# Optimization experiments

Hardware: AMD Instinct MI355X
Metric: run time of the kernel (lower is better)

## Reference

```python
import jax, jax.numpy as jnp
import numpy as np

VOCAB = 50000
D = 128      # word_embedding_size
H = 64       # attention_hidden_dim


def _doc_embed(words, emb_table, w_self, b_self):
    """words: (..., W) int -> (..., D) via tanh self-attention pooling over words."""
    we = emb_table[words]                                # (..., W, D)
    scores = jnp.tanh(we @ w_self + b_self)              # (..., W, 1)
    wgt = jax.nn.softmax(scores, axis=-2)                # softmax over word dim
    return jnp.sum(wgt * we, axis=-2)                    # (..., D)


def _attention(reviews_emb, query_emb, Wq, bq, w_red):
    """reviews_emb: (B,R,D), query_emb: (B,1,D) -> (B,D)."""
    B = query_emb.shape[0]
    pq = jnp.tanh(query_emb.reshape(B, D) @ Wq + bq)     # (B, D*H)
    pq = pq.reshape(B, D, H)
    s = jnp.einsum('brd,bdh->brh', reviews_emb, pq)      # (B,R,H)
    r = s @ w_red                                        # (B,R,1)
    w = jax.nn.softmax(r, axis=1)                        # softmax over reviews
    return jnp.sum(w * reviews_emb, axis=1)              # (B,D)


def setup_inputs() -> dict:
    key = jax.random.key(0)
    ks = jax.random.split(key, 9)
    B, R, W = 256, 20, 100
    user = jax.random.randint(ks[0], (B, R, W), 0, VOCAB)
    item = jax.random.randint(ks[1], (B, R, W), 0, VOCAB)
    query = jax.random.randint(ks[2], (B, W), 0, VOCAB)
    emb_table = jax.random.normal(ks[3], (VOCAB, D), dtype=jnp.float32) * 0.01
    w_self = jax.random.normal(ks[4], (D, 1), dtype=jnp.float32) * (1.0 / np.sqrt(D))
    b_self = jax.random.uniform(ks[5], (1,), dtype=jnp.float32, maxval=0.01)
    Wq = jax.random.normal(ks[6], (D, D * H), dtype=jnp.float32) * (1.0 / np.sqrt(D))
    bq = jax.random.uniform(ks[7], (D * H,), dtype=jnp.float32, maxval=0.01)
    w_red = jax.random.normal(ks[8], (H, 1), dtype=jnp.float32) * (1.0 / np.sqrt(H))
    pf = jnp.float32(0.5)  # personalized_factor
    return {"user_reviews_words": user, "item_reviews_words": item, "query": query,
            "emb_table": emb_table, "w_self": w_self, "b_self": b_self,
            "Wq": Wq, "bq": bq, "w_red": w_red, "pf": pf}


def reference(user_reviews_words, item_reviews_words, query,
              emb_table, w_self, b_self, Wq, bq, w_red, pf):
    # mode == 'test'
    user_emb = _doc_embed(user_reviews_words, emb_table, w_self, b_self)   # (B,R,D)
    item_emb = _doc_embed(item_reviews_words, emb_table, w_self, b_self)   # (B,R,D)
    q_emb = _doc_embed(query[:, None, :], emb_table, w_self, b_self)       # (B,1,D)
    user_entity = _attention(user_emb, q_emb, Wq, bq, w_red)               # (B,D)
    item_entity = _attention(item_emb, q_emb, Wq, bq, w_red)               # (B,D)
    personalized = user_entity + pf * q_emb[:, 0, :]
    return (personalized, item_entity)
```

## Files before the change

### kernel.cpp

```cpp
#include <hip/hip_runtime.h>
#include <math.h>

#define D 128
#define H 64
#define W 100
#define R 20
#define NB 256
#define NDOC_UI (NB * R)
#define VOCAB 50000

__device__ __forceinline__ float fast_tanh(float x) {
    float u = __expf(2.0f * x);
    return 1.0f - 2.0f * __builtin_amdgcn_rcpf(1.0f + u);
}
__device__ __forceinline__ float fast_exp_tanh(float x) {
    return __expf(fast_tanh(x));
}

__device__ __forceinline__ unsigned short f2bf(float f) {
    unsigned int b = __float_as_uint(f);
    b += 0x7fffu + ((b >> 16) & 1u);
    return (unsigned short)(b >> 16);
}

__global__ __launch_bounds__(256) void vocab_prep_kernel(
    const float* __restrict__ emb, const float* __restrict__ w_self,
    const float* __restrict__ b_self,
    ushort* __restrict__ emb_bf, float* __restrict__ evocab)
{
    int tid = threadIdx.x, lane32 = tid & 31, grp = tid >> 5;
    int row = blockIdx.x * 8 + grp;
    float4 v   = ((const float4*)emb)[row * 32 + lane32];
    float4 ws4 = ((const float4*)w_self)[lane32];
    float p = v.x * ws4.x + v.y * ws4.y + v.z * ws4.z + v.w * ws4.w;
    p += __shfl_xor(p, 16, 64);
    p += __shfl_xor(p, 8, 64);
    p += __shfl_xor(p, 4, 64);
    p += __shfl_xor(p, 2, 64);
    p += __shfl_xor(p, 1, 64);
    float e = __expf(tanhf(p + b_self[0]));
    if (lane32 == 0) evocab[row] = e;
    ushort4 u;
    u.x = f2bf(v.x * e); u.y = f2bf(v.y * e);
    u.z = f2bf(v.z * e); u.w = f2bf(v.w * e);
    ((ushort4*)emb_bf)[row * 32 + lane32] = u;
}

__global__ __launch_bounds__(256) void doc_embed_bf16_kernel(
    const int* __restrict__ user_w, const int* __restrict__ item_w,
    const int* __restrict__ query_w,
    const ushort* __restrict__ emb_bf, const float* __restrict__ evocab,
    float* __restrict__ user_emb, float* __restrict__ item_emb,
    float* __restrict__ q_emb)
{
    int tid    = threadIdx.x;
    int lane32 = tid & 31;
    int grp    = tid >> 5;
    int doc    = blockIdx.x * 8 + grp;

    const int* wp; float* outp;
    if (doc < NDOC_UI)        { wp = user_w + doc * W;               outp = user_emb + doc * D; }
    else if (doc < 2*NDOC_UI) { int t = doc - NDOC_UI;   wp = item_w  + t * W; outp = item_emb + t * D; }
    else                      { int t = doc - 2*NDOC_UI; wp = query_w + t * W; outp = q_emb    + t * D; }

    int wreg[4];
    #pragma unroll
    for (int k = 0; k < 4; ++k) {
        int idx = k * 32 + lane32;
        wreg[k] = wp[idx > W - 1 ? W - 1 : idx];
    }

    float ep = 0.f;
    #pragma unroll
    for (int k = 0; k < 4; ++k) {
        float e = evocab[wreg[k]];
        if (k < 3 || lane32 < 4) ep += e;
    }
    ep += __shfl_xor(ep, 16, 64);
    ep += __shfl_xor(ep, 8, 64);
    ep += __shfl_xor(ep, 4, 64);
    ep += __shfl_xor(ep, 2, 64);
    ep += __shfl_xor(ep, 1, 64);
    float inv = 1.f / ep;

    int permbase = (tid & 32) << 2;
    int sub      = lane32 >> 4;
    int quad     = lane32 & 15;

    float acc[8];
    #pragma unroll
    for (int j = 0; j < 8; ++j) acc[j] = 0.f;

    const uint4* ebf4 = (const uint4*)emb_bf;

    #pragma unroll
    for (int k = 0; k < 3; ++k) {
        #pragma unroll
        for (int hc = 0; hc < 2; ++hc) {
            int wid[8]; uint4 v[8];
            #pragma unroll
            for (int j = 0; j < 8; ++j) {
                int src = (hc * 8 + j) * 2 + sub;
                wid[j] = __builtin_amdgcn_ds_bpermute(permbase | (src << 2), wreg[k]);
            }
            #pragma unroll
            for (int j = 0; j < 8; ++j)
                v[j] = ebf4[(size_t)(unsigned)wid[j] * 16 + quad];
            #pragma unroll
            for (int j = 0; j < 8; ++j) {
                uint4 x = v[j];
                acc[0] += __uint_as_float(x.x << 16);
                acc[1] += __uint_as_float(x.x & 0xffff0000u);
                acc[2] += __uint_as_float(x.y << 16);
                acc[3] += __uint_as_float(x.y & 0xffff0000u);
                acc[4] += __uint_as_float(x.z << 16);
                acc[5] += __uint_as_float(x.z & 0xffff0000u);
                acc[6] += __uint_as_float(x.w << 16);
                acc[7] += __uint_as_float(x.w & 0xffff0000u);
            }
        }
    }
    {
        int wid[2]; uint4 v[2];
        #pragma unroll
        for (int j = 0; j < 2; ++j) {
            int src = j * 2 + sub;
            wid[j] = __builtin_amdgcn_ds_bpermute(permbase | (src << 2), wreg[3]);
        }
        #pragma unroll
        for (int j = 0; j < 2; ++j)
            v[j] = ebf4[(size_t)(unsigned)wid[j] * 16 + quad];
        #pragma unroll
        for (int j = 0; j < 2; ++j) {
            uint4 x = v[j];
            acc[0] += __uint_as_float(x.x << 16);
            acc[1] += __uint_as_float(x.x & 0xffff0000u);
            acc[2] += __uint_as_float(x.y << 16);
            acc[3] += __uint_as_float(x.y & 0xffff0000u);
            acc[4] += __uint_as_float(x.z << 16);
            acc[5] += __uint_as_float(x.z & 0xffff0000u);
            acc[6] += __uint_as_float(x.w << 16);
            acc[7] += __uint_as_float(x.w & 0xffff0000u);
        }
    }

    #pragma unroll
    for (int j = 0; j < 8; ++j) acc[j] += __shfl_xor(acc[j], 16, 64);

    if (lane32 < 16) {
        float4 o0 = make_float4(acc[0]*inv, acc[1]*inv, acc[2]*inv, acc[3]*inv);
        float4 o1 = make_float4(acc[4]*inv, acc[5]*inv, acc[6]*inv, acc[7]*inv);
        ((float4*)outp)[quad * 2]     = o0;
        ((float4*)outp)[quad * 2 + 1] = o1;
    }
}

__global__ __launch_bounds__(256, 7) void doc_embed_fp32_kernel(
    const int* __restrict__ user_w, const int* __restrict__ item_w,
    const int* __restrict__ query_w,
    const float* __restrict__ emb, const float* __restrict__ w_self,
    const float* __restrict__ b_self,
    float* __restrict__ user_emb, float* __restrict__ item_emb,
    float* __restrict__ q_emb)
{
    int tid    = threadIdx.x;
    int lane32 = tid & 31;
    int grp    = tid >> 5;
    int doc    = blockIdx.x * 8 + grp;

    const int* wp; float* outp;
    if (doc < NDOC_UI)        { wp = user_w + doc * W;               outp = user_emb + doc * D; }
    else if (doc < 2*NDOC_UI) { int t = doc - NDOC_UI;   wp = item_w  + t * W; outp = item_emb + t * D; }
    else                      { int t = doc - 2*NDOC_UI; wp = query_w + t * W; outp = q_emb    + t * D; }

    int wreg[4];
    #pragma unroll
    for (int k = 0; k < 4; ++k) {
        int idx = k * 32 + lane32;
        wreg[k] = wp[idx > W - 1 ? W - 1 : idx];
    }

    float4 ws4 = ((const float4*)w_self)[lane32];
    float  bs  = b_self[0];
    const float4* emb4 = (const float4*)emb;
    int permbase = (tid & 32) * 4;

    float4 acc  = make_float4(0.f, 0.f, 0.f, 0.f);
    float  esum = 0.f;

    #pragma unroll
    for (int c = 0; c < 10; ++c) {
        int word[10];
        #pragma unroll
        for (int j = 0; j < 10; ++j) {
            int w = c * 10 + j;
            word[j] = __builtin_amdgcn_ds_bpermute(permbase | ((w & 31) * 4),
                                                   wreg[w >> 5]);
        }
        float4 v[10];
        #pragma unroll
        for (int j = 0; j < 10; ++j)
            v[j] = emb4[(size_t)word[j] * 32 + lane32];

        #pragma unroll
        for (int j = 0; j < 10; ++j) {
            float p = v[j].x * ws4.x + v[j].y * ws4.y + v[j].z * ws4.z + v[j].w * ws4.w;
            p += __shfl_xor(p, 16, 64);
            p += __shfl_xor(p, 8, 64);
            p += __shfl_xor(p, 4, 64);
            p += __shfl_xor(p, 2, 64);
            p += __shfl_xor(p, 1, 64);
            float e = fast_exp_tanh(p + bs);
            esum += e;
            acc.x += e * v[j].x;
            acc.y += e * v[j].y;
            acc.z += e * v[j].z;
            acc.w += e * v[j].w;
        }
    }

    float inv = 1.0f / esum;
    acc.x *= inv; acc.y *= inv; acc.z *= inv; acc.w *= inv;
    ((float4*)outp)[lane32] = acc;
}

__global__ __launch_bounds__(256) void pv_kernel(
    const float* __restrict__ q_emb, const float* __restrict__ Wq,
    const float* __restrict__ bq, const float* __restrict__ w_red,
    float* __restrict__ pv)
{
    __shared__ __align__(16) float qs[64 * 132];
    __shared__ __align__(16) float Wb[128 * 68];

    int dd  = blockIdx.x;
    int m0g = blockIdx.y * 64;
    int tid = threadIdx.x;

    {
        int rrow = tid >> 4;
        int f4   = tid & 15;
        #pragma unroll
        for (int pass = 0; pass < 4; ++pass) {
            int m = pass * 16 + rrow;
            float4 vq = ((const float4*)q_emb)[(m0g + m) * 32 + f4];
            *(float4*)&qs[m * 132 + f4 * 4] = vq;
        }
        #pragma unroll
        for (int pass = 0; pass < 8; ++pass) {
            int k = pass * 16 + rrow;
            float4 vw = ((const float4*)Wq)[k * 2048 + dd * 16 + f4];
            *(float4*)&Wb[k * 68 + f4 * 4] = vw;
        }
    }
    __syncthreads();

    int nthr = tid & 7;
    int mthr = tid >> 3;
    int n0 = nthr * 8;
    int m0 = mthr * 2;

    float acc[2][8];
    #pragma unroll
    for (int i = 0; i < 2; ++i)
        #pragma unroll
        for (int j = 0; j < 8; ++j) acc[i][j] = 0.f;

    for (int k = 0; k < 128; ++k) {
        float4 b0 = *(const float4*)&Wb[k * 68 + n0];
        float4 b1 = *(const float4*)&Wb[k * 68 + n0 + 4];
        float a0 = qs[(m0 + 0) * 132 + k];
        float a1 = qs[(m0 + 1) * 132 + k];
        float bv[8] = {b0.x, b0.y, b0.z, b0.w, b1.x, b1.y, b1.z, b1.w};
        #pragma unroll
        for (int j = 0; j < 8; ++j) {
            acc[0][j] += a0 * bv[j];
            acc[1][j] += a1 * bv[j];
        }
    }

    float4 bqa = ((const float4*)bq)[dd * 16 + nthr * 2];
    float4 bqb = ((const float4*)bq)[dd * 16 + nthr * 2 + 1];
    float4 wra = ((const float4*)w_red)[nthr * 2];
    float4 wrb = ((const float4*)w_red)[nthr * 2 + 1];
    float bqv[8] = {bqa.x, bqa.y, bqa.z, bqa.w, bqb.x, bqb.y, bqb.z, bqb.w};
    float wrv[8] = {wra.x, wra.y, wra.z, wra.w, wrb.x, wrb.y, wrb.z, wrb.w};

    #pragma unroll
    for (int i = 0; i < 2; ++i) {
        float s = 0.f;
        #pragma unroll
        for (int j = 0; j < 8; ++j)
            s += fast_tanh(acc[i][j] + bqv[j]) * wrv[j];
        s += __shfl_xor(s, 1, 64);
        s += __shfl_xor(s, 2, 64);
        s += __shfl_xor(s, 4, 64);
        if (nthr == 0) pv[(m0g + m0 + i) * 128 + dd] = s;
    }
}

__global__ __launch_bounds__(256) void attn_kernel(
    const float* __restrict__ user_emb, const float* __restrict__ item_emb,
    const float* __restrict__ q_emb, const float* __restrict__ pv,
    const float* __restrict__ pf, float* __restrict__ out)
{
    __shared__ float rev[R * 129];
    __shared__ float pvl[D];
    __shared__ float sc[R];

    int b   = blockIdx.x;
    int set = blockIdx.y;
    const float* revg = (set == 0 ? user_emb : item_emb) + b * R * D;
    int tid = threadIdx.x;

    for (int idx = tid; idx < R * D; idx += 256)
        rev[(idx >> 7) * 129 + (idx & 127)] = revg[idx];
    if (tid < D) pvl[tid] = pv[b * D + tid];
    __syncthreads();

    if (tid < R) {
        float s = 0.f;
        const float* row = &rev[tid * 129];
        #pragma unroll 16
        for (int k = 0; k < D; ++k) s += row[k] * pvl[k];
        sc[tid] = s;
    }
    __syncthreads();

    float m = -1e30f;
    for (int r = 0; r < R; ++r) m = fmaxf(m, sc[r]);
    float sum = 0.f;
    for (int r = 0; r < R; ++r) sum += __expf(sc[r] - m);
    float inv = 1.f / sum;

    if (tid < D) {
        float acc = 0.f;
        for (int r = 0; r < R; ++r)
            acc += __expf(sc[r] - m) * inv * rev[r * 129 + tid];
        if (set == 0) {
            acc += pf[0] * q_emb[b * D + tid];
            out[b * D + tid] = acc;
        } else {
            out[NB * D + b * D + tid] = acc;
        }
    }
}

extern "C" void kernel_launch(void* const* d_in, const int* in_sizes, int n_in,
                              void* d_out, int out_size, void* d_ws, size_t ws_size,
                              hipStream_t stream) {
    const int*   user_w  = (const int*)d_in[0];
    const int*   item_w  = (const int*)d_in[1];
    const int*   query_w = (const int*)d_in[2];
    const float* emb     = (const float*)d_in[3];
    const float* w_self  = (const float*)d_in[4];
    const float* b_self  = (const float*)d_in[5];
    const float* Wq      = (const float*)d_in[6];
    const float* bq      = (const float*)d_in[7];
    const float* w_red   = (const float*)d_in[8];
    const float* pf      = (const float*)d_in[9];

    float* ws       = (float*)d_ws;
    float* user_emb = ws;
    float* item_emb = user_emb + NDOC_UI * D;
    float* q_emb    = item_emb + NDOC_UI * D;
    float* pv       = q_emb    + NB * D;
    float* evocab   = pv       + NB * D;
    ushort* emb_bf  = (ushort*)(evocab + VOCAB);
    float* out      = (float*)d_out;

    const size_t need_fast =
        (size_t)(2 * NDOC_UI * D + 2 * NB * D + VOCAB) * sizeof(float)
        + (size_t)VOCAB * D * sizeof(ushort);

    if (ws_size >= need_fast) {
        vocab_prep_kernel<<<VOCAB / 8, 256, 0, stream>>>(
            emb, w_self, b_self, emb_bf, evocab);
        doc_embed_bf16_kernel<<<(2 * NDOC_UI + NB) / 8, 256, 0, stream>>>(
            user_w, item_w, query_w, emb_bf, evocab, user_emb, item_emb, q_emb);
    } else {
        doc_embed_fp32_kernel<<<(2 * NDOC_UI + NB) / 8, 256, 0, stream>>>(
            user_w, item_w, query_w, emb, w_self, b_self, user_emb, item_emb, q_emb);
    }
    pv_kernel<<<dim3(128, 4), 256, 0, stream>>>(q_emb, Wq, bq, w_red, pv);
    attn_kernel<<<dim3(NB, 2), 256, 0, stream>>>(user_emb, item_emb, q_emb, pv, pf, out);
}
```

Baseline: 151.9 us.

## Retile pv GEMM with register-blocked q rows and widen doc-embed gather batches

The doc-embed kernel now runs 128-thread blocks of four docs each and gathers words in five batches of ten, replacing the uneven 8/8/2 batching so more row loads are in flight per wave. The pv kernel no longer stages q_emb in shared memory. Each thread streams eight q rows from global memory with register prefetch and computes an 8x4 output tile, halving the grid in y and covering 128 rows per block. This cuts LDS traffic and raises arithmetic per Wq tile load, at the cost of more registers and uncoalesced per-thread q loads.

```diff
diff --git a/kernel.cpp b/kernel.cpp
--- a/kernel.cpp
+++ b/kernel.cpp
@@ -46,7 +46,7 @@
     ((ushort4*)emb_bf)[row * 32 + lane32] = u;
 }
 
-__global__ __launch_bounds__(256) void doc_embed_bf16_kernel(
+__global__ __launch_bounds__(128) void doc_embed_bf16_kernel(
     const int* __restrict__ user_w, const int* __restrict__ item_w,
     const int* __restrict__ query_w,
     const ushort* __restrict__ emb_bf, const float* __restrict__ evocab,
@@ -56,7 +56,7 @@
     int tid    = threadIdx.x;
     int lane32 = tid & 31;
     int grp    = tid >> 5;
-    int doc    = blockIdx.x * 8 + grp;
+    int doc    = blockIdx.x * 4 + grp;
 
     const int* wp; float* outp;
     if (doc < NDOC_UI)        { wp = user_w + doc * W;               outp = user_emb + doc * D; }
@@ -94,44 +94,20 @@
     const uint4* ebf4 = (const uint4*)emb_bf;
 
     #pragma unroll
-    for (int k = 0; k < 3; ++k) {
-        #pragma unroll
-        for (int hc = 0; hc < 2; ++hc) {
-            int wid[8]; uint4 v[8];
-            #pragma unroll
-            for (int j = 0; j < 8; ++j) {
-                int src = (hc * 8 + j) * 2 + sub;
-                wid[j] = __builtin_amdgcn_ds_bpermute(permbase | (src << 2), wreg[k]);
-            }
-            #pragma unroll
-            for (int j = 0; j < 8; ++j)
-                v[j] = ebf4[(size_t)(unsigned)wid[j] * 16 + quad];
-            #pragma unroll
-            for (int j = 0; j < 8; ++j) {
-                uint4 x = v[j];
-                acc[0] += __uint_as_float(x.x << 16);
-                acc[1] += __uint_as_float(x.x & 0xffff0000u);
-                acc[2] += __uint_as_float(x.y << 16);
-                acc[3] += __uint_as_float(x.y & 0xffff0000u);
-                acc[4] += __uint_as_float(x.z << 16);
-                acc[5] += __uint_as_float(x.z & 0xffff0000u);
-                acc[6] += __uint_as_float(x.w << 16);
-                acc[7] += __uint_as_float(x.w & 0xffff0000u);
-            }
-        }
-    }
-    {
-        int wid[2]; uint4 v[2];
-        #pragma unroll
-        for (int j = 0; j < 2; ++j) {
-            int src = j * 2 + sub;
-            wid[j] = __builtin_amdgcn_ds_bpermute(permbase | (src << 2), wreg[3]);
-        }
-        #pragma unroll
-        for (int j = 0; j < 2; ++j)
+    for (int c = 0; c < 5; ++c) {
+        int wid[10]; uint4 v[10];
+        #pragma unroll
+        for (int j = 0; j < 10; ++j) {
+            int s = c * 10 + j;
+            int lane_src = ((2 * s) & 31) | sub;
+            wid[j] = __builtin_amdgcn_ds_bpermute(permbase | (lane_src << 2),
+                                                  wreg[s >> 4]);
+        }
+        #pragma unroll
+        for (int j = 0; j < 10; ++j)
             v[j] = ebf4[(size_t)(unsigned)wid[j] * 16 + quad];
         #pragma unroll
-        for (int j = 0; j < 2; ++j) {
+        for (int j = 0; j < 10; ++j) {
             uint4 x = v[j];
             acc[0] += __uint_as_float(x.x << 16);
             acc[1] += __uint_as_float(x.x & 0xffff0000u);
@@ -229,22 +205,15 @@
     const float* __restrict__ bq, const float* __restrict__ w_red,
     float* __restrict__ pv)
 {
-    __shared__ __align__(16) float qs[64 * 132];
     __shared__ __align__(16) float Wb[128 * 68];
 
     int dd  = blockIdx.x;
-    int m0g = blockIdx.y * 64;
+    int m0g = blockIdx.y * 128;
     int tid = threadIdx.x;
 
     {
         int rrow = tid >> 4;
         int f4   = tid & 15;
-        #pragma unroll
-        for (int pass = 0; pass < 4; ++pass) {
-            int m = pass * 16 + rrow;
-            float4 vq = ((const float4*)q_emb)[(m0g + m) * 32 + f4];
-            *(float4*)&qs[m * 132 + f4 * 4] = vq;
-        }
         #pragma unroll
         for (int pass = 0; pass < 8; ++pass) {
             int k = pass * 16 + rrow;
@@ -254,47 +223,58 @@
     }
     __syncthreads();
 
-    int nthr = tid & 7;
-    int mthr = tid >> 3;
-    int n0 = nthr * 8;
-    int m0 = mthr * 2;
-
-    float acc[2][8];
-    #pragma unroll
-    for (int i = 0; i < 2; ++i)
-        #pragma unroll
-        for (int j = 0; j < 8; ++j) acc[i][j] = 0.f;
-
-    for (int k = 0; k < 128; ++k) {
-        float4 b0 = *(const float4*)&Wb[k * 68 + n0];
-        float4 b1 = *(const float4*)&Wb[k * 68 + n0 + 4];
-        float a0 = qs[(m0 + 0) * 132 + k];
-        float a1 = qs[(m0 + 1) * 132 + k];
-        float bv[8] = {b0.x, b0.y, b0.z, b0.w, b1.x, b1.y, b1.z, b1.w};
-        #pragma unroll
-        for (int j = 0; j < 8; ++j) {
-            acc[0][j] += a0 * bv[j];
-            acc[1][j] += a1 * bv[j];
-        }
-    }
-
-    float4 bqa = ((const float4*)bq)[dd * 16 + nthr * 2];
-    float4 bqb = ((const float4*)bq)[dd * 16 + nthr * 2 + 1];
-    float4 wra = ((const float4*)w_red)[nthr * 2];
-    float4 wrb = ((const float4*)w_red)[nthr * 2 + 1];
-    float bqv[8] = {bqa.x, bqa.y, bqa.z, bqa.w, bqb.x, bqb.y, bqb.z, bqb.w};
-    float wrv[8] = {wra.x, wra.y, wra.z, wra.w, wrb.x, wrb.y, wrb.z, wrb.w};
-
-    #pragma unroll
-    for (int i = 0; i < 2; ++i) {
-        float s = 0.f;
-        #pragma unroll
-        for (int j = 0; j < 8; ++j)
-            s += fast_tanh(acc[i][j] + bqv[j]) * wrv[j];
+    int nthr = tid & 15;
+    int mthr = tid >> 4;
+    int n0 = nthr * 4;
+    const float4* q4 = (const float4*)q_emb;
+    int mbase = (m0g + mthr * 8) * 32;
+
+    float acc[8][4];
+    #pragma unroll
+    for (int i = 0; i < 8; ++i)
+        #pragma unroll
+        for (int j = 0; j < 4; ++j) acc[i][j] = 0.f;
+
+    float4 qa[8], qb[8];
+    #pragma unroll
+    for (int i = 0; i < 8; ++i) qa[i] = q4[mbase + i * 32];
+
+    for (int k4 = 0; k4 < 32; ++k4) {
+        if (k4 < 31) {
+            #pragma unroll
+            for (int i = 0; i < 8; ++i) qb[i] = q4[mbase + i * 32 + k4 + 1];
+        }
+        #pragma unroll
+        for (int kk = 0; kk < 4; ++kk) {
+            float4 wv = *(const float4*)&Wb[(k4 * 4 + kk) * 68 + n0];
+            #pragma unroll
+            for (int i = 0; i < 8; ++i) {
+                float a = (kk == 0) ? qa[i].x : (kk == 1) ? qa[i].y
+                        : (kk == 2) ? qa[i].z : qa[i].w;
+                acc[i][0] += a * wv.x;
+                acc[i][1] += a * wv.y;
+                acc[i][2] += a * wv.z;
+                acc[i][3] += a * wv.w;
+            }
+        }
+        #pragma unroll
+        for (int i = 0; i < 8; ++i) qa[i] = qb[i];
+    }
+
+    float4 bqv = ((const float4*)bq)[dd * 16 + nthr];
+    float4 wrv = ((const float4*)w_red)[nthr];
+
+    #pragma unroll
+    for (int i = 0; i < 8; ++i) {
+        float s = fast_tanh(acc[i][0] + bqv.x) * wrv.x
+                + fast_tanh(acc[i][1] + bqv.y) * wrv.y
+                + fast_tanh(acc[i][2] + bqv.z) * wrv.z
+                + fast_tanh(acc[i][3] + bqv.w) * wrv.w;
         s += __shfl_xor(s, 1, 64);
         s += __shfl_xor(s, 2, 64);
         s += __shfl_xor(s, 4, 64);
-        if (nthr == 0) pv[(m0g + m0 + i) * 128 + dd] = s;
+        s += __shfl_xor(s, 8, 64);
+        if (nthr == 0) pv[(m0g + mthr * 8 + i) * 128 + dd] = s;
     }
 }
 
@@ -375,12 +355,12 @@
     if (ws_size >= need_fast) {
         vocab_prep_kernel<<<VOCAB / 8, 256, 0, stream>>>(
             emb, w_self, b_self, emb_bf, evocab);
-        doc_embed_bf16_kernel<<<(2 * NDOC_UI + NB) / 8, 256, 0, stream>>>(
+        doc_embed_bf16_kernel<<<(2 * NDOC_UI + NB) / 4, 128, 0, stream>>>(
             user_w, item_w, query_w, emb_bf, evocab, user_emb, item_emb, q_emb);
     } else {
         doc_embed_fp32_kernel<<<(2 * NDOC_UI + NB) / 8, 256, 0, stream>>>(
             user_w, item_w, query_w, emb, w_self, b_self, user_emb, item_emb, q_emb);
     }
-    pv_kernel<<<dim3(128, 4), 256, 0, stream>>>(q_emb, Wq, bq, w_red, pv);
+    pv_kernel<<<dim3(128, 2), 256, 0, stream>>>(q_emb, Wq, bq, w_red, pv);
     attn_kernel<<<dim3(NB, 2), 256, 0, stream>>>(user_emb, item_emb, q_emb, pv, pf, out);
 }
```

After: 152.7 us. About the same (+0.6%).
